# Performance work log

Measured on AMD Instinct MI355X. Metric: run time of the kernel, lower is better.

The kernel has to match this reference:

```python
import jax, jax.numpy as jnp
import numpy as np

N = 100_000   # nodes
E = 3_200_000 # edges
G = 512       # graphs in batch
H = 64        # hidden dim
C = 7         # num classes


def setup_inputs() -> dict:
    key = jax.random.key(0)
    ks = jax.random.split(key, 8)
    x = jax.random.normal(ks[0], (N, 1), dtype=jnp.float32)
    edge_index = jax.random.randint(ks[1], (2, E), 0, N, dtype=jnp.int32)
    batch = jnp.sort(jax.random.randint(ks[2], (N,), 0, G, dtype=jnp.int32))
    W1 = jax.random.normal(ks[3], (1, H), dtype=jnp.float32) / np.sqrt(1.0)
    b1 = jnp.zeros((H,), jnp.float32)
    W2 = jax.random.normal(ks[4], (H, H), dtype=jnp.float32) / np.sqrt(H)
    b2 = jnp.zeros((H,), jnp.float32)
    fW1 = jax.random.normal(ks[5], (H, 32), dtype=jnp.float32) / np.sqrt(H)
    fb1 = jnp.zeros((32,), jnp.float32)
    fW2 = jax.random.normal(ks[6], (32, C), dtype=jnp.float32) / np.sqrt(32.0)
    fb2 = jnp.zeros((C,), jnp.float32)
    return {"x": x, "edge_index": edge_index, "batch": batch,
            "W1": W1, "b1": b1, "W2": W2, "b2": b2,
            "fW1": fW1, "fb1": fb1, "fW2": fW2, "fb2": fb2}


def reference(x, edge_index, batch, W1, b1, W2, b2, fW1, fb1, fW2, fb2):
    # GCNConv with self-loops and symmetric normalization (PyG defaults).
    src, dst = edge_index[0], edge_index[1]
    loop = jnp.arange(N, dtype=src.dtype)
    s = jnp.concatenate([src, loop])  # [E+N]
    d = jnp.concatenate([dst, loop])
    deg = jax.ops.segment_sum(jnp.ones(s.shape, jnp.float32), d, num_segments=N)
    dis = jnp.where(deg > 0, jax.lax.rsqrt(jnp.maximum(deg, 1.0)), 0.0)
    norm = dis[s] * dis[d]  # [E+N]

    def gcn(h, W, b):
        h = h @ W                                   # [N, out]
        msg = norm[:, None] * h[s]                  # gather + scale
        return jax.ops.segment_sum(msg, d, num_segments=N) + b

    # Dropout is identity in eval/reference mode.
    h = jax.nn.relu(gcn(x, W1, b1))
    h = jax.nn.relu(gcn(h, W2, b2))

    # global_mean_pool over graph assignment `batch`
    cnt = jax.ops.segment_sum(jnp.ones((N,), jnp.float32), batch, num_segments=G)
    pooled = jax.ops.segment_sum(h, batch, num_segments=G) / jnp.maximum(cnt, 1.0)[:, None]

    h = jax.nn.relu(pooled @ fW1 + fb1)
    return h @ fW2 + fb2  # [G, C] logits
```

## Files before the change

### kernel.cpp

```cpp
#include <hip/hip_runtime.h>

#define N_NODES 100000
#define N_EDGES 3200000
#define G_GRAPHS 512
#define HDIM 64
#define CBSH 11
#define CBN 2048
#define NCB ((N_NODES + CBN - 1) / CBN)
#define EPW 4096
#define NWG ((N_EDGES + EPW - 1) / EPW)
#define EPT (EPW / 256)
#define SPL 8
#define RTHR 512
#define WPS ((NWG + SPL - 1) / SPL)
#define MAXROWS 25

__global__ __launch_bounds__(256) void kzp(const float* __restrict__ W1,
                                           const float* __restrict__ b1,
                                           const float* __restrict__ W2,
                                           float* __restrict__ dt, int* __restrict__ meta,
                                           float* __restrict__ pw1, float* __restrict__ pb1,
                                           int* __restrict__ pdidx,
                                           float* __restrict__ w2p, float* __restrict__ tabs,
                                           int* __restrict__ deg, float* __restrict__ q,
                                           float* __restrict__ pool, int* __restrict__ cnt,
                                           float* __restrict__ histA, float* __restrict__ histW) {
    int tid = threadIdx.x;
    if (blockIdx.x < 16) {
        __shared__ float ts[HDIM], srt[HDIM];
        __shared__ int isnew[HDIM], rr[HDIM], kpermS[HDIM], rankS[HDIM];
        __shared__ int ndS;
        if (tid < HDIM) {
            float w1 = W1[tid], bb = b1[tid];
            ts[tid] = (w1 != 0.f) ? (-bb / w1) : -1e30f;
        }
        __syncthreads();
        if (tid < HDIM) {
            float tj = ts[tid];
            int r = 0;
            for (int i = 0; i < HDIM; ++i) {
                float ti = ts[i];
                if (ti < tj || (ti == tj && i < tid)) r++;
            }
            rr[tid] = r;
            srt[r] = tj;
            kpermS[r] = tid;
        }
        __syncthreads();
        if (tid < HDIM) {
            int r = rr[tid];
            isnew[r] = (r == 0) || (srt[r] != srt[r - 1]);
        }
        __syncthreads();
        if (tid < HDIM) {
            int r = rr[tid];
            int didx = 0;
            for (int qq = 0; qq <= r; ++qq) didx += isnew[qq];
            didx -= 1;
            rankS[tid] = didx;
            if (blockIdx.x == 0 && isnew[r]) dt[didx] = srt[r];
        }
        if (tid == 0) {
            int nd = 0;
            for (int qq = 0; qq < HDIM; ++qq) nd += isnew[qq];
            ndS = nd;
            if (blockIdx.x == 0) {
                int nw = 0;
                for (int qq = 0; qq < HDIM; ++qq) nw |= (b1[qq] != 0.f) ? 1 : 0;
                meta[0] = nd; meta[1] = nw;
            }
        }
        __syncthreads();
        int nd = ndS;
        if (blockIdx.x == 0 && tid < HDIM) {
            int pj = kpermS[tid];
            pw1[tid] = W1[pj]; pb1[tid] = b1[pj]; pdidx[tid] = rankS[pj];
        }
        int i = blockIdx.x * 256 + tid;
        if (i < HDIM * HDIM) {
            int r = i >> 6, j = i & 63;
            w2p[i] = W2[kpermS[r] * HDIM + j];
        }
        if (nd <= 6 && i < (1 + 4 * nd) * HDIM) {
            int r = i >> 6, j = i & 63;
            float acc = 0.f;
            if (r == 0) {
                for (int jj = 0; jj < HDIM; ++jj)
                    if (W1[jj] == 0.f) acc += fmaxf(b1[jj], 0.f) * W2[jj * HDIM + j];
            } else {
                int qq = (r - 1) >> 2, c = (r - 1) & 3;
                for (int jj = 0; jj < HDIM; ++jj) {
                    if (rankS[jj] != qq) continue;
                    float w1 = W1[jj], bb = b1[jj];
                    float wr = W2[jj * HDIM + j];
                    if      (c == 0 && w1 > 0.f) acc += w1 * wr;
                    else if (c == 1 && w1 < 0.f) acc += w1 * wr;
                    else if (c == 2 && w1 > 0.f) acc += bb * wr;
                    else if (c == 3 && w1 < 0.f) acc += bb * wr;
                }
            }
            tabs[i] = acc;
        }
    }
    size_t gtid = (size_t)blockIdx.x * blockDim.x + threadIdx.x;
    size_t stride = (size_t)gridDim.x * blockDim.x;
    for (size_t i = gtid; i < N_NODES; i += stride) { deg[i] = 0; q[i] = 0.f; }
    for (size_t i = gtid; i < G_GRAPHS * HDIM; i += stride) pool[i] = 0.f;
    for (size_t i = gtid; i < G_GRAPHS; i += stride) cnt[i] = 0;
    size_t nh = (size_t)7 * N_NODES;
    for (size_t i = gtid; i < nh; i += stride) { histA[i] = 0.f; histW[i] = 0.f; }
}

__global__ __launch_bounds__(256) void kB2(const int* __restrict__ src,
                                           const int* __restrict__ dst,
                                           unsigned* __restrict__ sorted,
                                           int* __restrict__ wgcnt,
                                           int* __restrict__ wgpre) {
    __shared__ int hist[NCB];
    __shared__ int basep[NCB];
    __shared__ unsigned sbuf[EPW];
    int tid = threadIdx.x;
    int w = blockIdx.x;
    int e0 = w * EPW;
    int ecnt = min(EPW, N_EDGES - e0);
    if (tid < NCB) hist[tid] = 0;
    __syncthreads();
    int dreg[EPT], sreg[EPT];
    const uint4* dst4 = reinterpret_cast<const uint4*>(dst + e0);
    const uint4* src4 = reinterpret_cast<const uint4*>(src + e0);
    #pragma unroll
    for (int t = 0; t < EPT / 4; ++t) {
        int v = t * 256 + tid;
        if (v * 4 < ecnt) {
            uint4 dv = dst4[v];
            uint4 sv = src4[v];
            int base = v * 4;
            dreg[t*4+0] = (base+0 < ecnt) ? (int)dv.x : -1;
            dreg[t*4+1] = (base+1 < ecnt) ? (int)dv.y : -1;
            dreg[t*4+2] = (base+2 < ecnt) ? (int)dv.z : -1;
            dreg[t*4+3] = (base+3 < ecnt) ? (int)dv.w : -1;
            sreg[t*4+0] = (int)sv.x; sreg[t*4+1] = (int)sv.y;
            sreg[t*4+2] = (int)sv.z; sreg[t*4+3] = (int)sv.w;
            #pragma unroll
            for (int k = 0; k < 4; ++k)
                if (dreg[t*4+k] >= 0) atomicAdd(&hist[dreg[t*4+k] >> CBSH], 1);
        } else {
            dreg[t*4+0] = dreg[t*4+1] = dreg[t*4+2] = dreg[t*4+3] = -1;
        }
    }
    __syncthreads();
    if (tid < 64) {
        int h = (tid < NCB) ? hist[tid] : 0;
        int v = h;
        #pragma unroll
        for (int off = 1; off < 64; off <<= 1) {
            int uu = __shfl_up(v, off, 64);
            if (tid >= off) v += uu;
        }
        if (tid < NCB) {
            basep[tid] = v - h;
            wgcnt[w * NCB + tid] = h;
            wgpre[w * NCB + tid] = v - h;
        }
    }
    __syncthreads();
    #pragma unroll
    for (int t = 0; t < EPT; ++t) {
        int d = dreg[t];
        if (d >= 0) {
            int b = d >> CBSH;
            int pos = atomicAdd(&basep[b], 1);
            sbuf[pos] = ((unsigned)sreg[t] << CBSH) | (unsigned)(d & (CBN - 1));
        }
    }
    __syncthreads();
    uint4* out4 = reinterpret_cast<uint4*>(sorted + e0);
    const uint4* sb4 = reinterpret_cast<const uint4*>(sbuf);
    int nv4 = ecnt >> 2;
    for (int i = tid; i < nv4; i += 256) out4[i] = sb4[i];
    for (int i = (nv4 << 2) + tid; i < ecnt; i += 256) sorted[e0 + i] = sbuf[i];
}

#define FOR_RUNS(BODY)                                                        \
    {                                                                         \
        int wv = tid >> 6, ln = tid & 63;                                     \
        int w0 = sp * WPS, w1e = min(w0 + WPS, NWG);                          \
        for (int w = w0 + wv; w < w1e; w += (RTHR / 64)) {                    \
            int st = w * EPW + wgpre[w * NCB + b];                            \
            int cb = wgcnt[w * NCB + b];                                      \
            for (int i = ln; i < cb; i += 64) { unsigned ww = sorted[st + i]; BODY } \
        }                                                                     \
    }

__global__ __launch_bounds__(RTHR) void kdeg2(const unsigned* __restrict__ sorted,
                                              const int* __restrict__ wgcnt,
                                              const int* __restrict__ wgpre,
                                              int* __restrict__ deg) {
    __shared__ int dcnt[CBN];
    int b = blockIdx.x / SPL, sp = blockIdx.x % SPL, tid = threadIdx.x;
    for (int i = tid; i < CBN; i += RTHR) dcnt[i] = 0;
    __syncthreads();
    FOR_RUNS( atomicAdd(&dcnt[ww & (CBN - 1)], 1); )
    __syncthreads();
    int nb = b * CBN;
    for (int i = tid; i < CBN; i += RTHR) {
        int c = dcnt[i];
        if (c && nb + i < N_NODES) atomicAdd(&deg[nb + i], c);
    }
}

__global__ void k2_dis(const int* __restrict__ deg, const float* __restrict__ x,
                       float* __restrict__ dis, float* __restrict__ u) {
    int n = blockIdx.x * blockDim.x + threadIdx.x;
    if (n < N_NODES) {
        float d = rsqrtf((float)(deg[n] + 1));
        dis[n] = d;
        u[n] = d * x[n];
    }
}

__global__ __launch_bounds__(RTHR) void kq3(const unsigned* __restrict__ sorted,
                                            const int* __restrict__ wgcnt,
                                            const int* __restrict__ wgpre,
                                            const float* __restrict__ u,
                                            float* __restrict__ q) {
    __shared__ float qL[CBN];
    int b = blockIdx.x / SPL, sp = blockIdx.x % SPL, tid = threadIdx.x;
    for (int i = tid; i < CBN; i += RTHR) qL[i] = 0.f;
    __syncthreads();
    FOR_RUNS( atomicAdd(&qL[ww & (CBN - 1)], u[ww >> CBSH]); )
    __syncthreads();
    int nb = b * CBN;
    for (int i = tid; i < CBN; i += RTHR) {
        float v = qL[i];
        if (v != 0.f && nb + i < N_NODES) atomicAdd(&q[nb + i], v);
    }
}

__global__ void k3b(const int* __restrict__ deg, const float* __restrict__ x,
                    const float* __restrict__ dis, const float* __restrict__ q,
                    float2* __restrict__ ad) {
    int n = blockIdx.x * blockDim.x + threadIdx.x;
    if (n < N_NODES) {
        float d = dis[n];
        ad[n] = make_float2(d * q[n] + x[n] / (float)(deg[n] + 1), d);
    }
}

template<int LO, int HI, int PLANES>
__global__ __launch_bounds__(RTHR) void khist3t(const unsigned* __restrict__ sorted,
                                                const int* __restrict__ wgcnt,
                                                const int* __restrict__ wgpre,
                                                const float2* __restrict__ ad,
                                                const float* __restrict__ dt,
                                                const int* __restrict__ meta,
                                                float* __restrict__ histA,
                                                float* __restrict__ histW) {
    __shared__ float bA[PLANES * CBN];
    __shared__ float dtS[8];
    int nd = meta[0], needW = meta[1];
    if (nd < LO || nd > HI) return;
    int b = blockIdx.x / SPL, sp = blockIdx.x % SPL, tid = threadIdx.x;
    if (tid < 8) dtS[tid] = (tid < nd) ? dt[tid] : 3.4e38f;
    int nb = b * CBN;
    int nparts = 1 + (needW ? 1 : 0);
    for (int part = 0; part < nparts; ++part) {
        for (int i = tid; i < (nd + 1) * CBN; i += RTHR) bA[i] = 0.f;
        __syncthreads();
        FOR_RUNS(
            float2 t = ad[ww >> CBSH];
            float a = t.x;
            int k = 0;
            _Pragma("unroll")
            for (int qq = 0; qq < HI; ++qq) k += (dtS[qq] < a) ? 1 : 0;
            atomicAdd(&bA[k * CBN + (ww & (CBN - 1))], part ? t.y : t.y * a);
        )
        __syncthreads();
        float* H = part ? histW : histA;
        for (int k = 0; k <= nd; ++k)
            for (int i = tid; i < CBN; i += RTHR) {
                float v = bA[k * CBN + i];
                if (v != 0.f && nb + i < N_NODES)
                    atomicAdd(&H[(size_t)k * N_NODES + nb + i], v);
            }
        __syncthreads();
    }
}

__global__ __launch_bounds__(256) void knode_fast(
        const float* __restrict__ histA, const float* __restrict__ histW,
        const int* __restrict__ meta, const float* __restrict__ dt,
        const float* __restrict__ tabs,
        const float2* __restrict__ ad, const float* __restrict__ b2,
        const int* __restrict__ batch,
        float* __restrict__ pool, int* __restrict__ cnt) {
    __shared__ float h2s[HDIM * 65];
    __shared__ float tabL[MAXROWS * HDIM];
    __shared__ float dtS[8];
    int nd = meta[0], needW = meta[1];
    if (nd > 6) return;
    int tid = threadIdx.x;
    int nl = tid & 63, cg = tid >> 6;
    int n0 = blockIdx.x * 64;
    int nvalid = min(64, N_NODES - n0);
    int n = n0 + min(nl, nvalid - 1);
    float2 adn = ad[n];
    float a = adn.x, d = adn.y;
    int c16 = cg * 16;

    int nrows = 1 + 4 * nd;
    for (int i = tid; i < nrows * HDIM; i += 256) tabL[i] = tabs[i];
    if (tid < nd) dtS[tid] = dt[tid];
    __syncthreads();
    float TA = 0.f, TW = 0.f;
    for (int bq = 0; bq <= nd; ++bq) {
        TA += histA[(size_t)bq * N_NODES + n];
        if (needW) TW += histW[(size_t)bq * N_NODES + n];
    }
    int k = 0;
    for (int q = 0; q < nd; ++q) k += (dtS[q] < a) ? 1 : 0;
    float z[16];
    #pragma unroll
    for (int t = 0; t < 16; ++t) z[t] = b2[c16 + t];
    float d2 = d * d;
    float cC = d * TW + d2;
    #pragma unroll
    for (int t = 0; t < 16; ++t) z[t] += cC * tabL[c16 + t];
    float run = 0.f, runW = 0.f;
    for (int q = 0; q < nd; ++q) {
        run += histA[(size_t)q * N_NODES + n];
        if (needW) runW += histW[(size_t)q * N_NODES + n];
        bool act = (q < k);
        float cWp = d * (TA - run) + (act ? d2 * a : 0.f);
        float cWm = d * run + (act ? 0.f : d2 * a);
        float cBp = d * (TW - runW) + (act ? d2 : 0.f);
        float cBm = d * runW + (act ? 0.f : d2);
        int base = (1 + 4 * q) * HDIM + c16;
        #pragma unroll
        for (int t = 0; t < 16; ++t)
            z[t] += cWp * tabL[base + t] + cWm * tabL[base + HDIM + t]
                  + cBp * tabL[base + 2 * HDIM + t] + cBm * tabL[base + 3 * HDIM + t];
    }
    #pragma unroll
    for (int t = 0; t < 16; ++t) h2s[nl * 65 + c16 + t] = fmaxf(z[t], 0.f);

    __syncthreads();
    int i0 = cg * 16, i1 = min(i0 + 16, nvalid);
    float accP = 0.f; int gcur = -1, runC = 0;
    for (int i = i0; i < i1; ++i) {
        int g = batch[n0 + i];
        float v = h2s[i * 65 + nl];
        if (g != gcur) {
            if (gcur >= 0) {
                atomicAdd(&pool[(size_t)gcur * HDIM + nl], accP);
                if (nl == 0) atomicAdd(&cnt[gcur], runC);
            }
            gcur = g; accP = 0.f; runC = 0;
        }
        accP += v; ++runC;
    }
    if (gcur >= 0) {
        atomicAdd(&pool[(size_t)gcur * HDIM + nl], accP);
        if (nl == 0) atomicAdd(&cnt[gcur], runC);
    }
}

__global__ __launch_bounds__(256) void knode_gen(
        const int* __restrict__ meta,
        const float* __restrict__ pw1, const float* __restrict__ pb1,
        const float* __restrict__ w2p,
        const float2* __restrict__ ad, const float* __restrict__ b2,
        const int* __restrict__ batch,
        const unsigned* __restrict__ sorted, const int* __restrict__ wgcnt,
        const int* __restrict__ wgpre,
        float* __restrict__ pool, int* __restrict__ cnt) {
    int nd = meta[0];
    if (nd <= 6) return;
    __shared__ float h2s[HDIM * 65];
    int tid = threadIdx.x;
    int nl = tid & 63, cg = tid >> 6;
    int n0 = blockIdx.x * 64;
    int nvalid = min(64, N_NODES - n0);
    int n = n0 + min(nl, nvalid - 1);
    float2 adn = ad[n];
    float a = adn.x, d = adn.y;
    int c16 = cg * 16;
    float areg[HDIM];
    #pragma unroll
    for (int jj = 0; jj < HDIM; ++jj) areg[jj] = 0.f;
    int b = n >> CBSH;
    int myld = n & (CBN - 1);
    for (int w = 0; w < NWG; ++w) {
        int st = w * EPW + wgpre[w * NCB + b];
        int cb = wgcnt[w * NCB + b];
        for (int i = 0; i < cb; ++i) {
            unsigned ww = sorted[st + i];
            if ((int)(ww & (CBN - 1)) == myld) {
                float2 t = ad[ww >> CBSH];
                #pragma unroll
                for (int jj = 0; jj < HDIM; ++jj)
                    areg[jj] += t.y * fmaxf(t.x * pw1[jj] + pb1[jj], 0.f);
            }
        }
    }
    #pragma unroll
    for (int jj = 0; jj < HDIM; ++jj)
        areg[jj] = d * areg[jj] + d * d * fmaxf(a * pw1[jj] + pb1[jj], 0.f);
    float z[16];
    #pragma unroll
    for (int t = 0; t < 16; ++t) z[t] = b2[c16 + t];
    for (int jj = 0; jj < HDIM; ++jj) {
        float av = areg[jj];
        #pragma unroll
        for (int t = 0; t < 16; ++t) z[t] += av * w2p[jj * HDIM + c16 + t];
    }
    #pragma unroll
    for (int t = 0; t < 16; ++t) h2s[nl * 65 + c16 + t] = fmaxf(z[t], 0.f);

    __syncthreads();
    int i0 = cg * 16, i1 = min(i0 + 16, nvalid);
    float accP = 0.f; int gcur = -1, runC = 0;
    for (int i = i0; i < i1; ++i) {
        int g = batch[n0 + i];
        float v = h2s[i * 65 + nl];
        if (g != gcur) {
            if (gcur >= 0) {
                atomicAdd(&pool[(size_t)gcur * HDIM + nl], accP);
                if (nl == 0) atomicAdd(&cnt[gcur], runC);
            }
            gcur = g; accP = 0.f; runC = 0;
        }
        accP += v; ++runC;
    }
    if (gcur >= 0) {
        atomicAdd(&pool[(size_t)gcur * HDIM + nl], accP);
        if (nl == 0) atomicAdd(&cnt[gcur], runC);
    }
}

__global__ void k7_mlp(const float* __restrict__ pool, const int* __restrict__ cnt,
                       const float* __restrict__ fW1, const float* __restrict__ fb1,
                       const float* __restrict__ fW2, const float* __restrict__ fb2,
                       float* __restrict__ out) {
    __shared__ float p[HDIM];
    __shared__ float tt[32];
    int g = blockIdx.x;
    int tid = threadIdx.x;
    float c = fmaxf((float)cnt[g], 1.f);
    p[tid] = pool[g * HDIM + tid] / c;
    __syncthreads();
    if (tid < 32) {
        float acc = fb1[tid];
        #pragma unroll
        for (int j = 0; j < HDIM; ++j) acc += p[j] * fW1[j * 32 + tid];
        tt[tid] = fmaxf(acc, 0.f);
    }
    __syncthreads();
    if (tid < 7) {
        float acc = fb2[tid];
        #pragma unroll
        for (int i = 0; i < 32; ++i) acc += tt[i] * fW2[i * 7 + tid];
        out[g * 7 + tid] = acc;
    }
}

__global__ void kf1_deg(const int* __restrict__ dst, int* __restrict__ deg) {
    int e = blockIdx.x * blockDim.x + threadIdx.x;
    if (e < N_EDGES) atomicAdd(&deg[dst[e]], 1);
}
__global__ void kf2_dis(const int* __restrict__ deg, const float* __restrict__ x,
                        float* __restrict__ dis, float* __restrict__ agg1) {
    int n = blockIdx.x * blockDim.x + threadIdx.x;
    if (n < N_NODES) {
        float d = (float)(deg[n] + 1);
        dis[n] = rsqrtf(d);
        agg1[n] = x[n] / d;
    }
}
__global__ void kf3_agg1(const int* __restrict__ src, const int* __restrict__ dst,
                         const float* __restrict__ dis, const float* __restrict__ x,
                         float* __restrict__ agg1) {
    int e = blockIdx.x * blockDim.x + threadIdx.x;
    if (e < N_EDGES) {
        int s = src[e], d = dst[e];
        atomicAdd(&agg1[d], dis[s] * dis[d] * x[s]);
    }
}
__global__ void kf4_agg2init(const float* __restrict__ agg1, const float* __restrict__ dis,
                             const float* __restrict__ W1, const float* __restrict__ b1,
                             float* __restrict__ agg2) {
    int i = blockIdx.x * blockDim.x + threadIdx.x;
    if (i < N_NODES * HDIM) {
        int n = i >> 6, j = i & 63;
        float h = fmaxf(agg1[n] * W1[j] + b1[j], 0.f);
        float r = dis[n];
        agg2[i] = r * r * h;
    }
}
__global__ void kf5_edge(const int* __restrict__ src, const int* __restrict__ dst,
                         const float* __restrict__ dis, const float* __restrict__ agg1,
                         const float* __restrict__ W1, const float* __restrict__ b1,
                         float* __restrict__ agg2) {
    int t = blockIdx.x * blockDim.x + threadIdx.x;
    int e = t >> 6, j = t & 63;
    if (e < N_EDGES) {
        int s = src[e], d = dst[e];
        float w = dis[s] * dis[d];
        float h = fmaxf(agg1[s] * W1[j] + b1[j], 0.f);
        atomicAdd(&agg2[d * HDIM + j], w * h);
    }
}
__global__ void kf6_pool(const float* __restrict__ agg2, const float* __restrict__ W2,
                         const float* __restrict__ b2, const int* __restrict__ batch,
                         float* __restrict__ pool, int* __restrict__ cnt) {
    __shared__ float w2s[HDIM * HDIM];
    int tid = threadIdx.x;
    for (int i = tid; i < HDIM * HDIM; i += blockDim.x) w2s[i] = W2[i];
    __syncthreads();
    int lane = tid & 63, wid = tid >> 6;
    int nwaves = gridDim.x * 4;
    for (int n = blockIdx.x * 4 + wid; n < N_NODES; n += nwaves) {
        float av  = agg2[n * HDIM + lane];
        float acc = b2[lane];
        #pragma unroll
        for (int k = 0; k < HDIM; ++k)
            acc += __shfl(av, k, 64) * w2s[k * HDIM + lane];
        acc = fmaxf(acc, 0.f);
        int g = batch[n];
        atomicAdd(&pool[g * HDIM + lane], acc);
        if (lane == 0) atomicAdd(&cnt[g], 1);
    }
}

extern "C" void kernel_launch(void* const* d_in, const int* in_sizes, int n_in,
                              void* d_out, int out_size, void* d_ws, size_t ws_size,
                              hipStream_t stream) {
    const float* x    = (const float*)d_in[0];
    const int*   ei   = (const int*)  d_in[1];
    const int*   batch= (const int*)  d_in[2];
    const float* W1   = (const float*)d_in[3];
    const float* b1   = (const float*)d_in[4];
    const float* W2   = (const float*)d_in[5];
    const float* b2   = (const float*)d_in[6];
    const float* fW1  = (const float*)d_in[7];
    const float* fb1  = (const float*)d_in[8];
    const float* fW2  = (const float*)d_in[9];
    const float* fb2  = (const float*)d_in[10];
    const int* src = ei;
    const int* dst = ei + N_EDGES;
    float* out = (float*)d_out;

    size_t off = 0;
    auto take = [&](size_t bytes) { size_t o = off; off = (off + bytes + 255) & ~(size_t)255; return o; };
    char* base = (char*)d_ws;
    int*     deg   = (int*)     (base + take((size_t)N_NODES * 4));
    float*   pool  = (float*)   (base + take((size_t)G_GRAPHS * HDIM * 4));
    int*     cnt   = (int*)     (base + take((size_t)G_GRAPHS * 4));
    float*   dis   = (float*)   (base + take((size_t)N_NODES * 4));
    float*   u     = (float*)   (base + take((size_t)N_NODES * 4));
    float*   q     = (float*)   (base + take((size_t)N_NODES * 4));
    float2*  ad    = (float2*)  (base + take((size_t)N_NODES * 8));
    float*   dt    = (float*)   (base + take(HDIM * 4));
    int*     meta  = (int*)     (base + take(64));
    float*   pw1   = (float*)   (base + take(HDIM * 4));
    float*   pb1   = (float*)   (base + take(HDIM * 4));
    int*     pdidx = (int*)     (base + take(HDIM * 4));
    float*   w2p   = (float*)   (base + take(HDIM * HDIM * 4));
    float*   tabs  = (float*)   (base + take((size_t)MAXROWS * HDIM * 4));
    int*     wgcnt = (int*)     (base + take((size_t)NWG * NCB * 4));
    int*     wgpre = (int*)     (base + take((size_t)NWG * NCB * 4));
    size_t sorted_off = off;
    unsigned* sorted = (unsigned*)(base + take((size_t)N_EDGES * 4));
    float*   histA = (float*)   (base + take((size_t)7 * N_NODES * 4));
    float*   histW = (float*)   (base + take((size_t)7 * N_NODES * 4));
    size_t need_fast = off;

    if (ws_size >= need_fast) {
        kzp   <<<1024, 256, 0, stream>>>(W1, b1, W2, dt, meta, pw1, pb1, pdidx, w2p, tabs,
                                         deg, q, pool, cnt, histA, histW);
        kB2   <<<NWG, 256, 0, stream>>>(src, dst, sorted, wgcnt, wgpre);
        kdeg2 <<<NCB * SPL, RTHR, 0, stream>>>(sorted, wgcnt, wgpre, deg);
        k2_dis<<<(N_NODES + 255) / 256, 256, 0, stream>>>(deg, x, dis, u);
        kq3   <<<NCB * SPL, RTHR, 0, stream>>>(sorted, wgcnt, wgpre, u, q);
        k3b   <<<(N_NODES + 255) / 256, 256, 0, stream>>>(deg, x, dis, q, ad);
        khist3t<0, 1, 2><<<NCB * SPL, RTHR, 0, stream>>>(sorted, wgcnt, wgpre, ad, dt, meta, histA, histW);
        khist3t<2, 6, 7><<<NCB * SPL, RTHR, 0, stream>>>(sorted, wgcnt, wgpre, ad, dt, meta, histA, histW);
        knode_fast<<<(N_NODES + 63) / 64, 256, 0, stream>>>(histA, histW, meta, dt, tabs,
                                                            ad, b2, batch, pool, cnt);
        knode_gen <<<(N_NODES + 63) / 64, 256, 0, stream>>>(meta, pw1, pb1, w2p, ad, b2, batch,
                                                            sorted, wgcnt, wgpre, pool, cnt);
        k7_mlp<<<G_GRAPHS, 64, 0, stream>>>(pool, cnt, fW1, fb1, fW2, fb2, out);
    } else {
        float* agg1 = u;
        float* agg2 = (float*)(base + sorted_off);
        hipMemsetAsync(deg, 0, (size_t)N_NODES * 4, stream);
        hipMemsetAsync(pool, 0, (size_t)G_GRAPHS * HDIM * 4 + 1024, stream);
        kf1_deg<<<(N_EDGES + 255) / 256, 256, 0, stream>>>(dst, deg);
        kf2_dis<<<(N_NODES + 255) / 256, 256, 0, stream>>>(deg, x, dis, agg1);
        kf3_agg1<<<(N_EDGES + 255) / 256, 256, 0, stream>>>(src, dst, dis, x, agg1);
        kf4_agg2init<<<(N_NODES * HDIM + 255) / 256, 256, 0, stream>>>(agg1, dis, W1, b1, agg2);
        int k5_blocks = (int)(((long long)N_EDGES * HDIM + 255) / 256);
        kf5_edge<<<k5_blocks, 256, 0, stream>>>(src, dst, dis, agg1, W1, b1, agg2);
        kf6_pool<<<2048, 256, 0, stream>>>(agg2, W2, b2, batch, pool, cnt);
        k7_mlp<<<G_GRAPHS, 64, 0, stream>>>(pool, cnt, fW1, fb1, fW2, fb2, out);
    }
}
```

Before: 135.1 us.

## Fuse per-node epilogues into scatter kernels via last-block counters and merge kernel variants

```diff
diff --git a/kernel.cpp b/kernel.cpp
--- a/kernel.cpp
+++ b/kernel.cpp
@@ -20,11 +20,11 @@
                                            const float* __restrict__ W2,
                                            float* __restrict__ dt, int* __restrict__ meta,
                                            float* __restrict__ pw1, float* __restrict__ pb1,
-                                           int* __restrict__ pdidx,
                                            float* __restrict__ w2p, float* __restrict__ tabs,
                                            int* __restrict__ deg, float* __restrict__ q,
                                            float* __restrict__ pool, int* __restrict__ cnt,
-                                           float* __restrict__ histA, float* __restrict__ histW) {
+                                           float* __restrict__ histA, float* __restrict__ histW,
+                                           int* __restrict__ ctrD, int* __restrict__ ctrQ) {
     int tid = threadIdx.x;
     if (blockIdx.x < 16) {
         __shared__ float ts[HDIM], srt[HDIM];
@@ -74,7 +74,7 @@
         int nd = ndS;
         if (blockIdx.x == 0 && tid < HDIM) {
             int pj = kpermS[tid];
-            pw1[tid] = W1[pj]; pb1[tid] = b1[pj]; pdidx[tid] = rankS[pj];
+            pw1[tid] = W1[pj]; pb1[tid] = b1[pj];
         }
         int i = blockIdx.x * 256 + tid;
         if (i < HDIM * HDIM) {
@@ -107,6 +107,7 @@
     for (size_t i = gtid; i < N_NODES; i += stride) { deg[i] = 0; q[i] = 0.f; }
     for (size_t i = gtid; i < G_GRAPHS * HDIM; i += stride) pool[i] = 0.f;
     for (size_t i = gtid; i < G_GRAPHS; i += stride) cnt[i] = 0;
+    for (size_t i = gtid; i < NCB; i += stride) { ctrD[i] = 0; ctrQ[i] = 0; }
     size_t nh = (size_t)7 * N_NODES;
     for (size_t i = gtid; i < nh; i += stride) { histA[i] = 0.f; histW[i] = 0.f; }
 }
@@ -195,8 +196,13 @@
 __global__ __launch_bounds__(RTHR) void kdeg2(const unsigned* __restrict__ sorted,
                                               const int* __restrict__ wgcnt,
                                               const int* __restrict__ wgpre,
-                                              int* __restrict__ deg) {
+                                              const float* __restrict__ x,
+                                              int* __restrict__ deg,
+                                              float* __restrict__ dis,
+                                              float* __restrict__ u,
+                                              int* __restrict__ ctrD) {
     __shared__ int dcnt[CBN];
+    __shared__ int isLast;
     int b = blockIdx.x / SPL, sp = blockIdx.x % SPL, tid = threadIdx.x;
     for (int i = tid; i < CBN; i += RTHR) dcnt[i] = 0;
     __syncthreads();
@@ -207,15 +213,20 @@
         int c = dcnt[i];
         if (c && nb + i < N_NODES) atomicAdd(&deg[nb + i], c);
     }
-}
-
-__global__ void k2_dis(const int* __restrict__ deg, const float* __restrict__ x,
-                       float* __restrict__ dis, float* __restrict__ u) {
-    int n = blockIdx.x * blockDim.x + threadIdx.x;
-    if (n < N_NODES) {
-        float d = rsqrtf((float)(deg[n] + 1));
-        dis[n] = d;
-        u[n] = d * x[n];
+    __threadfence();
+    __syncthreads();
+    if (tid == 0) isLast = (atomicAdd(&ctrD[b], 1) == SPL - 1) ? 1 : 0;
+    __syncthreads();
+    if (isLast) {
+        for (int i = tid; i < CBN; i += RTHR) {
+            int n = nb + i;
+            if (n < N_NODES) {
+                int dg = atomicAdd(&deg[n], 0);
+                float dn = rsqrtf((float)(dg + 1));
+                dis[n] = dn;
+                u[n] = dn * x[n];
+            }
+        }
     }
 }
 
@@ -223,8 +234,14 @@
                                             const int* __restrict__ wgcnt,
                                             const int* __restrict__ wgpre,
                                             const float* __restrict__ u,
-                                            float* __restrict__ q) {
+                                            const float* __restrict__ x,
+                                            const float* __restrict__ dis,
+                                            const int* __restrict__ deg,
+                                            float* __restrict__ q,
+                                            float2* __restrict__ ad,
+                                            int* __restrict__ ctrQ) {
     __shared__ float qL[CBN];
+    __shared__ int isLast;
     int b = blockIdx.x / SPL, sp = blockIdx.x % SPL, tid = threadIdx.x;
     for (int i = tid; i < CBN; i += RTHR) qL[i] = 0.f;
     __syncthreads();
@@ -235,31 +252,34 @@
         float v = qL[i];
         if (v != 0.f && nb + i < N_NODES) atomicAdd(&q[nb + i], v);
     }
-}
-
-__global__ void k3b(const int* __restrict__ deg, const float* __restrict__ x,
-                    const float* __restrict__ dis, const float* __restrict__ q,
-                    float2* __restrict__ ad) {
-    int n = blockIdx.x * blockDim.x + threadIdx.x;
-    if (n < N_NODES) {
-        float d = dis[n];
-        ad[n] = make_float2(d * q[n] + x[n] / (float)(deg[n] + 1), d);
-    }
-}
-
-template<int LO, int HI, int PLANES>
-__global__ __launch_bounds__(RTHR) void khist3t(const unsigned* __restrict__ sorted,
-                                                const int* __restrict__ wgcnt,
-                                                const int* __restrict__ wgpre,
-                                                const float2* __restrict__ ad,
-                                                const float* __restrict__ dt,
-                                                const int* __restrict__ meta,
-                                                float* __restrict__ histA,
-                                                float* __restrict__ histW) {
-    __shared__ float bA[PLANES * CBN];
+    __threadfence();
+    __syncthreads();
+    if (tid == 0) isLast = (atomicAdd(&ctrQ[b], 1) == SPL - 1) ? 1 : 0;
+    __syncthreads();
+    if (isLast) {
+        for (int i = tid; i < CBN; i += RTHR) {
+            int n = nb + i;
+            if (n < N_NODES) {
+                float qf = atomicAdd(&q[n], 0.f);
+                float dn = dis[n];
+                ad[n] = make_float2(dn * qf + x[n] / (float)(deg[n] + 1), dn);
+            }
+        }
+    }
+}
+
+__global__ __launch_bounds__(RTHR) void khist(const unsigned* __restrict__ sorted,
+                                              const int* __restrict__ wgcnt,
+                                              const int* __restrict__ wgpre,
+                                              const float2* __restrict__ ad,
+                                              const float* __restrict__ dt,
+                                              const int* __restrict__ meta,
+                                              float* __restrict__ histA,
+                                              float* __restrict__ histW) {
+    __shared__ float bA[7 * CBN];
     __shared__ float dtS[8];
     int nd = meta[0], needW = meta[1];
-    if (nd < LO || nd > HI) return;
+    if (nd > 6) return;
     int b = blockIdx.x / SPL, sp = blockIdx.x % SPL, tid = threadIdx.x;
     if (tid < 8) dtS[tid] = (tid < nd) ? dt[tid] : 3.4e38f;
     int nb = b * CBN;
@@ -272,7 +292,7 @@
             float a = t.x;
             int k = 0;
             _Pragma("unroll")
-            for (int qq = 0; qq < HI; ++qq) k += (dtS[qq] < a) ? 1 : 0;
+            for (int qq = 0; qq < 6; ++qq) k += (dtS[qq] < a) ? 1 : 0;
             atomicAdd(&bA[k * CBN + (ww & (CBN - 1))], part ? t.y : t.y * a);
         )
         __syncthreads();
@@ -287,86 +307,10 @@
     }
 }
 
-__global__ __launch_bounds__(256) void knode_fast(
+__global__ __launch_bounds__(256) void knode(
         const float* __restrict__ histA, const float* __restrict__ histW,
         const int* __restrict__ meta, const float* __restrict__ dt,
         const float* __restrict__ tabs,
-        const float2* __restrict__ ad, const float* __restrict__ b2,
-        const int* __restrict__ batch,
-        float* __restrict__ pool, int* __restrict__ cnt) {
-    __shared__ float h2s[HDIM * 65];
-    __shared__ float tabL[MAXROWS * HDIM];
-    __shared__ float dtS[8];
-    int nd = meta[0], needW = meta[1];
-    if (nd > 6) return;
-    int tid = threadIdx.x;
-    int nl = tid & 63, cg = tid >> 6;
-    int n0 = blockIdx.x * 64;
-    int nvalid = min(64, N_NODES - n0);
-    int n = n0 + min(nl, nvalid - 1);
-    float2 adn = ad[n];
-    float a = adn.x, d = adn.y;
-    int c16 = cg * 16;
-
-    int nrows = 1 + 4 * nd;
-    for (int i = tid; i < nrows * HDIM; i += 256) tabL[i] = tabs[i];
-    if (tid < nd) dtS[tid] = dt[tid];
-    __syncthreads();
-    float TA = 0.f, TW = 0.f;
-    for (int bq = 0; bq <= nd; ++bq) {
-        TA += histA[(size_t)bq * N_NODES + n];
-        if (needW) TW += histW[(size_t)bq * N_NODES + n];
-    }
-    int k = 0;
-    for (int q = 0; q < nd; ++q) k += (dtS[q] < a) ? 1 : 0;
-    float z[16];
-    #pragma unroll
-    for (int t = 0; t < 16; ++t) z[t] = b2[c16 + t];
-    float d2 = d * d;
-    float cC = d * TW + d2;
-    #pragma unroll
-    for (int t = 0; t < 16; ++t) z[t] += cC * tabL[c16 + t];
-    float run = 0.f, runW = 0.f;
-    for (int q = 0; q < nd; ++q) {
-        run += histA[(size_t)q * N_NODES + n];
-        if (needW) runW += histW[(size_t)q * N_NODES + n];
-        bool act = (q < k);
-        float cWp = d * (TA - run) + (act ? d2 * a : 0.f);
-        float cWm = d * run + (act ? 0.f : d2 * a);
-        float cBp = d * (TW - runW) + (act ? d2 : 0.f);
-        float cBm = d * runW + (act ? 0.f : d2);
-        int base = (1 + 4 * q) * HDIM + c16;
-        #pragma unroll
-        for (int t = 0; t < 16; ++t)
-            z[t] += cWp * tabL[base + t] + cWm * tabL[base + HDIM + t]
-                  + cBp * tabL[base + 2 * HDIM + t] + cBm * tabL[base + 3 * HDIM + t];
-    }
-    #pragma unroll
-    for (int t = 0; t < 16; ++t) h2s[nl * 65 + c16 + t] = fmaxf(z[t], 0.f);
-
-    __syncthreads();
-    int i0 = cg * 16, i1 = min(i0 + 16, nvalid);
-    float accP = 0.f; int gcur = -1, runC = 0;
-    for (int i = i0; i < i1; ++i) {
-        int g = batch[n0 + i];
-        float v = h2s[i * 65 + nl];
-        if (g != gcur) {
-            if (gcur >= 0) {
-                atomicAdd(&pool[(size_t)gcur * HDIM + nl], accP);
-                if (nl == 0) atomicAdd(&cnt[gcur], runC);
-            }
-            gcur = g; accP = 0.f; runC = 0;
-        }
-        accP += v; ++runC;
-    }
-    if (gcur >= 0) {
-        atomicAdd(&pool[(size_t)gcur * HDIM + nl], accP);
-        if (nl == 0) atomicAdd(&cnt[gcur], runC);
-    }
-}
-
-__global__ __launch_bounds__(256) void knode_gen(
-        const int* __restrict__ meta,
         const float* __restrict__ pw1, const float* __restrict__ pb1,
         const float* __restrict__ w2p,
         const float2* __restrict__ ad, const float* __restrict__ b2,
@@ -374,48 +318,92 @@
         const unsigned* __restrict__ sorted, const int* __restrict__ wgcnt,
         const int* __restrict__ wgpre,
         float* __restrict__ pool, int* __restrict__ cnt) {
-    int nd = meta[0];
-    if (nd <= 6) return;
     __shared__ float h2s[HDIM * 65];
+    __shared__ float tabL[MAXROWS * HDIM];
+    __shared__ float dtS[8];
     int tid = threadIdx.x;
     int nl = tid & 63, cg = tid >> 6;
     int n0 = blockIdx.x * 64;
     int nvalid = min(64, N_NODES - n0);
     int n = n0 + min(nl, nvalid - 1);
+    int nd = meta[0], needW = meta[1];
     float2 adn = ad[n];
     float a = adn.x, d = adn.y;
     int c16 = cg * 16;
-    float areg[HDIM];
-    #pragma unroll
-    for (int jj = 0; jj < HDIM; ++jj) areg[jj] = 0.f;
-    int b = n >> CBSH;
-    int myld = n & (CBN - 1);
-    for (int w = 0; w < NWG; ++w) {
-        int st = w * EPW + wgpre[w * NCB + b];
-        int cb = wgcnt[w * NCB + b];
-        for (int i = 0; i < cb; ++i) {
-            unsigned ww = sorted[st + i];
-            if ((int)(ww & (CBN - 1)) == myld) {
-                float2 t = ad[ww >> CBSH];
-                #pragma unroll
-                for (int jj = 0; jj < HDIM; ++jj)
-                    areg[jj] += t.y * fmaxf(t.x * pw1[jj] + pb1[jj], 0.f);
-            }
-        }
-    }
-    #pragma unroll
-    for (int jj = 0; jj < HDIM; ++jj)
-        areg[jj] = d * areg[jj] + d * d * fmaxf(a * pw1[jj] + pb1[jj], 0.f);
-    float z[16];
-    #pragma unroll
-    for (int t = 0; t < 16; ++t) z[t] = b2[c16 + t];
-    for (int jj = 0; jj < HDIM; ++jj) {
-        float av = areg[jj];
-        #pragma unroll
-        for (int t = 0; t < 16; ++t) z[t] += av * w2p[jj * HDIM + c16 + t];
-    }
-    #pragma unroll
-    for (int t = 0; t < 16; ++t) h2s[nl * 65 + c16 + t] = fmaxf(z[t], 0.f);
+
+    if (nd <= 6) {
+        int nrows = 1 + 4 * nd;
+        for (int i = tid; i < nrows * HDIM; i += 256) tabL[i] = tabs[i];
+        if (tid < nd) dtS[tid] = dt[tid];
+        __syncthreads();
+        float TA = 0.f, TW = 0.f;
+        for (int bq = 0; bq <= nd; ++bq) {
+            TA += histA[(size_t)bq * N_NODES + n];
+            if (needW) TW += histW[(size_t)bq * N_NODES + n];
+        }
+        int k = 0;
+        for (int q = 0; q < nd; ++q) k += (dtS[q] < a) ? 1 : 0;
+        float z[16];
+        #pragma unroll
+        for (int t = 0; t < 16; ++t) z[t] = b2[c16 + t];
+        float d2 = d * d;
+        float cC = d * TW + d2;
+        #pragma unroll
+        for (int t = 0; t < 16; ++t) z[t] += cC * tabL[c16 + t];
+        float run = 0.f, runW = 0.f;
+        for (int q = 0; q < nd; ++q) {
+            run += histA[(size_t)q * N_NODES + n];
+            if (needW) runW += histW[(size_t)q * N_NODES + n];
+            bool act = (q < k);
+            float cWp = d * (TA - run) + (act ? d2 * a : 0.f);
+            float cWm = d * run + (act ? 0.f : d2 * a);
+            float cBp = d * (TW - runW) + (act ? d2 : 0.f);
+            float cBm = d * runW + (act ? 0.f : d2);
+            int base = (1 + 4 * q) * HDIM + c16;
+            #pragma unroll
+            for (int t = 0; t < 16; ++t)
+                z[t] += cWp * tabL[base + t] + cWm * tabL[base + HDIM + t]
+                      + cBp * tabL[base + 2 * HDIM + t] + cBm * tabL[base + 3 * HDIM + t];
+        }
+        #pragma unroll
+        for (int t = 0; t < 16; ++t) h2s[nl * 65 + c16 + t] = fmaxf(z[t], 0.f);
+    } else {
+        float zz[16];
+        #pragma unroll
+        for (int t = 0; t < 16; ++t) zz[t] = 0.f;
+        int b = n >> CBSH;
+        int myld = n & (CBN - 1);
+        for (int w = 0; w < NWG; ++w) {
+            int st = w * EPW + wgpre[w * NCB + b];
+            int cb = wgcnt[w * NCB + b];
+            for (int i = 0; i < cb; ++i) {
+                unsigned ww = sorted[st + i];
+                if ((int)(ww & (CBN - 1)) == myld) {
+                    float2 t2 = ad[ww >> CBSH];
+                    #pragma unroll
+                    for (int t = 0; t < 16; ++t)
+                        zz[t] += t2.y * fmaxf(t2.x * pw1[c16 + t] + pb1[c16 + t], 0.f);
+                }
+            }
+        }
+        #pragma unroll
+        for (int t = 0; t < 16; ++t)
+            zz[t] = d * zz[t] + d * d * fmaxf(a * pw1[c16 + t] + pb1[c16 + t], 0.f);
+        #pragma unroll
+        for (int t = 0; t < 16; ++t) h2s[nl * 65 + c16 + t] = zz[t];
+        __syncthreads();
+        float z[16];
+        #pragma unroll
+        for (int t = 0; t < 16; ++t) z[t] = b2[c16 + t];
+        for (int jj = 0; jj < HDIM; ++jj) {
+            float av = h2s[nl * 65 + jj];
+            #pragma unroll
+            for (int t = 0; t < 16; ++t) z[t] += av * w2p[jj * HDIM + c16 + t];
+        }
+        __syncthreads();
+        #pragma unroll
+        for (int t = 0; t < 16; ++t) h2s[nl * 65 + c16 + t] = fmaxf(z[t], 0.f);
+    }
 
     __syncthreads();
     int i0 = cg * 16, i1 = min(i0 + 16, nvalid);
@@ -564,9 +552,10 @@
     int*     meta  = (int*)     (base + take(64));
     float*   pw1   = (float*)   (base + take(HDIM * 4));
     float*   pb1   = (float*)   (base + take(HDIM * 4));
-    int*     pdidx = (int*)     (base + take(HDIM * 4));
     float*   w2p   = (float*)   (base + take(HDIM * HDIM * 4));
     float*   tabs  = (float*)   (base + take((size_t)MAXROWS * HDIM * 4));
+    int*     ctrD  = (int*)     (base + take(NCB * 4));
+    int*     ctrQ  = (int*)     (base + take(NCB * 4));
     int*     wgcnt = (int*)     (base + take((size_t)NWG * NCB * 4));
     int*     wgpre = (int*)     (base + take((size_t)NWG * NCB * 4));
     size_t sorted_off = off;
@@ -576,19 +565,15 @@
     size_t need_fast = off;
 
     if (ws_size >= need_fast) {
-        kzp   <<<1024, 256, 0, stream>>>(W1, b1, W2, dt, meta, pw1, pb1, pdidx, w2p, tabs,
-                                         deg, q, pool, cnt, histA, histW);
+        kzp   <<<1024, 256, 0, stream>>>(W1, b1, W2, dt, meta, pw1, pb1, w2p, tabs,
+                                         deg, q, pool, cnt, histA, histW, ctrD, ctrQ);
         kB2   <<<NWG, 256, 0, stream>>>(src, dst, sorted, wgcnt, wgpre);
-        kdeg2 <<<NCB * SPL, RTHR, 0, stream>>>(sorted, wgcnt, wgpre, deg);
-        k2_dis<<<(N_NODES + 255) / 256, 256, 0, stream>>>(deg, x, dis, u);
-        kq3   <<<NCB * SPL, RTHR, 0, stream>>>(sorted, wgcnt, wgpre, u, q);
-        k3b   <<<(N_NODES + 255) / 256, 256, 0, stream>>>(deg, x, dis, q, ad);
-        khist3t<0, 1, 2><<<NCB * SPL, RTHR, 0, stream>>>(sorted, wgcnt, wgpre, ad, dt, meta, histA, histW);
-        khist3t<2, 6, 7><<<NCB * SPL, RTHR, 0, stream>>>(sorted, wgcnt, wgpre, ad, dt, meta, histA, histW);
-        knode_fast<<<(N_NODES + 63) / 64, 256, 0, stream>>>(histA, histW, meta, dt, tabs,
-                                                            ad, b2, batch, pool, cnt);
-        knode_gen <<<(N_NODES + 63) / 64, 256, 0, stream>>>(meta, pw1, pb1, w2p, ad, b2, batch,
-                                                            sorted, wgcnt, wgpre, pool, cnt);
+        kdeg2 <<<NCB * SPL, RTHR, 0, stream>>>(sorted, wgcnt, wgpre, x, deg, dis, u, ctrD);
+        kq3   <<<NCB * SPL, RTHR, 0, stream>>>(sorted, wgcnt, wgpre, u, x, dis, deg, q, ad, ctrQ);
+        khist <<<NCB * SPL, RTHR, 0, stream>>>(sorted, wgcnt, wgpre, ad, dt, meta, histA, histW);
+        knode <<<(N_NODES + 63) / 64, 256, 0, stream>>>(histA, histW, meta, dt, tabs,
+                                                        pw1, pb1, w2p, ad, b2, batch,
+                                                        sorted, wgcnt, wgpre, pool, cnt);
         k7_mlp<<<G_GRAPHS, 64, 0, stream>>>(pool, cnt, fW1, fb1, fW2, fb2, out);
     } else {
         float* agg1 = u;
```

Result: slower. 225.0 us (+66.5%).
